# Performance work log

Measured on AMD Instinct MI355X. Metric: run time of the kernel, lower is better.

## Reference

```python
import jax, jax.numpy as jnp
import numpy as np

STRIDES = (8, 16, 32, 64, 128)
IMG = 1024
NUM_CLS = 80
SHRINK_RATIO = 0.2
BIG = 1e7  # padding value for area of non-positive locations (matches tf.pad constant)


def _level_targets(boxes, labels, valid, stride):
    """Vectorized per-level target assignment.
    boxes: [B,M,4] float, labels: [B,M] int32, valid: [B,M] bool.
    Replaces the per-box tf.map_fn + dynamic pad + argmin + gather_nd with a
    dense masked area map and a single argmin/gather pass.
    """
    B, M, _ = boxes.shape
    fh = fw = IMG // stride
    HW = fh * fw
    # shrink_and_normalize_boxes: scale to level, shrink around center, clamp
    b = boxes / stride
    cx = (b[..., 0] + b[..., 2]) * 0.5
    cy = (b[..., 1] + b[..., 3]) * 0.5
    hw = (b[..., 2] - b[..., 0]) * 0.5 * SHRINK_RATIO
    hh = (b[..., 3] - b[..., 1]) * 0.5 * SHRINK_RATIO
    px1 = jnp.maximum(jnp.floor(cx - hw), 0.0)
    py1 = jnp.maximum(jnp.floor(cy - hh), 0.0)
    px2 = jnp.minimum(jnp.ceil(cx + hw), float(fw))
    py2 = jnp.minimum(jnp.ceil(cy + hh), float(fh))
    xs = jnp.arange(fw, dtype=jnp.float32)
    ys = jnp.arange(fh, dtype=jnp.float32)
    in_x = (xs[None, None, None, :] >= px1[:, :, None, None]) & (xs[None, None, None, :] < px2[:, :, None, None])
    in_y = (ys[None, None, :, None] >= py1[:, :, None, None]) & (ys[None, None, :, None] < py2[:, :, None, None])
    inside = in_x & in_y & valid[:, :, None, None]  # [B,M,fh,fw]
    area = (boxes[..., 2] - boxes[..., 0]) * (boxes[..., 3] - boxes[..., 1])  # [B,M]
    area_map = jnp.where(inside, area[:, :, None, None], BIG)  # [B,M,fh,fw]
    winner = jnp.argmin(area_map, axis=1).reshape(B, HW)  # min-area box per pixel
    win_area = jnp.min(area_map, axis=1).reshape(B, HW)
    pos = win_area < BIG  # pixel covered by at least one valid box
    posf = pos.astype(jnp.float32)
    wb = jnp.take_along_axis(boxes, winner[..., None], axis=1)  # [B,HW,4]
    wl = jnp.take_along_axis(labels, winner, axis=1)            # [B,HW]
    yy, xx = jnp.meshgrid(ys, xs, indexing='ij')
    sx = (xx.reshape(-1) + 0.5) * stride  # [HW] anchor-point x in image coords
    sy = (yy.reshape(-1) + 0.5) * stride
    l = sx[None, :] - wb[..., 0]
    t = sy[None, :] - wb[..., 1]
    r = wb[..., 2] - sx[None, :]
    btm = wb[..., 3] - sy[None, :]
    reg = jnp.stack([l, t, r, btm], axis=-1) / (4.0 * stride)  # [B,HW,4]
    eps = 1e-6
    cent = jnp.sqrt(
        jnp.clip(jnp.minimum(l, r) / jnp.maximum(jnp.maximum(l, r), eps), 0.0, 1.0)
        * jnp.clip(jnp.minimum(t, btm) / jnp.maximum(jnp.maximum(t, btm), eps), 0.0, 1.0))
    soft = jnp.where(pos, cent, 1.0)  # negatives padded with 1 (constant_values=1)
    cls_onehot = jax.nn.one_hot(wl, NUM_CLS, dtype=jnp.float32) * posf[..., None]
    cls_t = jnp.concatenate([cls_onehot, soft[..., None], posf[..., None]], axis=-1)  # [B,HW,C+2]
    reg_t = jnp.concatenate([reg * posf[..., None], soft[..., None], posf[..., None]], axis=-1)  # [B,HW,6]
    ind = jnp.where(pos, winner, -1).astype(jnp.int32)
    return cls_t, reg_t, ind


def setup_inputs():
    key = jax.random.key(0)
    B, M = 16, 100
    k1, k2, k3, k4, k5, k6 = jax.random.split(key, 6)
    w = jax.random.uniform(k1, (B, M)) * 240.0 + 16.0
    h = jax.random.uniform(k2, (B, M)) * 240.0 + 16.0
    cx = jax.random.uniform(k3, (B, M)) * (IMG - 260.0) + 130.0
    cy = jax.random.uniform(k4, (B, M)) * (IMG - 260.0) + 130.0
    labels = jax.random.randint(k5, (B, M), 0, NUM_CLS).astype(jnp.float32)
    x1 = cx - w * 0.5
    x2 = cx + w * 0.5
    y1 = cy - h * 0.5
    y2 = cy + h * 0.5
    # zero-pad trailing boxes per batch element (trim_zero_padding_boxes convention)
    n_valid = jax.random.randint(k6, (B,), 10, M + 1)
    valid = jnp.arange(M)[None, :] < n_valid[:, None]
    gt_boxes = jnp.stack([x1, y1, x2, y2, labels], axis=-1) * valid[..., None]
    return {"gt_boxes": gt_boxes.astype(jnp.float32)}


def reference(gt_boxes):
    boxes = gt_boxes[..., :4]
    labels = gt_boxes[..., 4].astype(jnp.int32)
    valid = jnp.sum(jnp.abs(boxes), axis=-1) > 0.0  # trim_zero_padding_boxes
    cls_all, reg_all, ind_all = [], [], []
    for stride in STRIDES:  # fixed 5 FPN levels
        c, r, i = _level_targets(boxes, labels, valid, stride)
        cls_all.append(c)
        reg_all.append(r)
        ind_all.append(i)
    cls_t = jnp.concatenate(cls_all, axis=1)   # [B, 21824, 82]
    reg_t = jnp.concatenate(reg_all, axis=1)   # [B, 21824, 6]
    ind_t = jnp.concatenate(ind_all, axis=1)[..., None]  # [B, 21824, 1]
    num_boxes = jnp.sum(valid.astype(jnp.int32), axis=1, keepdims=True)  # [B,1]
    return cls_t, reg_t, ind_t, num_boxes
```

## Files before the change

### kernel.cpp

```cpp
#include <hip/hip_runtime.h>
#include <stdint.h>

#define NCLS   80
#define HWTOT  21824
#define MBOX   100

#define REG_OFF 28633088ull
#define IND_OFF 30728192ull
#define NB_OFF  31077376ull

__global__ __launch_bounds__(256)
void sapd_targets(const float* __restrict__ gt, float* __restrict__ out)
{
    const int tid = threadIdx.x;
    const int c   = blockIdx.x;
    const int b   = blockIdx.y;

    int lvl, pix0, base;
    if      (c < 64) { lvl = 0; pix0 = c << 8;        base = 0;     }
    else if (c < 80) { lvl = 1; pix0 = (c - 64) << 8; base = 16384; }
    else if (c < 84) { lvl = 2; pix0 = (c - 80) << 8; base = 20480; }
    else if (c < 85) { lvl = 3; pix0 = 0;             base = 21504; }
    else             { lvl = 4; pix0 = 0;             base = 21760; }

    const int   l2fw   = 7 - lvl;
    const int   fw     = 1 << l2fw;
    const float fs     = (float)(8 << lvl);
    const int   chunkN = (lvl == 4) ? 64 : 256;

    const size_t rowbase = (size_t)b * HWTOT + base + pix0;

    __shared__ uint32_t sBB[MBOX];
    __shared__ float    sArea[MBOX];
    __shared__ int      sValid[MBOX];
    __shared__ float4   sBox[MBOX];
    __shared__ int      sLab[MBOX];
    __shared__ float2   sCull[MBOX];
    __shared__ int      sOrig[MBOX];
    __shared__ int      sN;
    __shared__ float4   sMeta[257];
    __shared__ float    rReg[256 * 4];

    if (tid < MBOX) {
        const float* g = gt + ((size_t)b * MBOX + tid) * 5;
        float x1 = g[0], y1 = g[1], x2 = g[2], y2 = g[3], lab = g[4];
        int valid = (fabsf(x1) + fabsf(y1) + fabsf(x2) + fabsf(y2)) > 0.0f;
        float area = (x2 - x1) * (y2 - y1);
        float bx1 = x1 / fs, by1 = y1 / fs, bx2 = x2 / fs, by2 = y2 / fs;
        float cx = (bx1 + bx2) * 0.5f, cy = (by1 + by2) * 0.5f;
        float hw = (bx2 - bx1) * 0.5f * 0.2f, hh = (by2 - by1) * 0.5f * 0.2f;
        float px1 = fmaxf(floorf(cx - hw), 0.0f);
        float py1 = fmaxf(floorf(cy - hh), 0.0f);
        float px2 = fminf(ceilf(cx + hw), (float)fw);
        float py2 = fminf(ceilf(cy + hh), (float)fw);
        uint32_t bb = (uint32_t)px1 | ((uint32_t)py1 << 8) |
                      ((uint32_t)px2 << 16) | ((uint32_t)py2 << 24);
        sBB[tid]    = bb;
        sArea[tid]  = area;
        sValid[tid] = valid;
        sBox[tid]   = make_float4(x1, y1, x2, y2);
        sLab[tid]   = (int)lab;
    }
    __syncthreads();

    if (lvl == 4 && tid == 64) {
        int cnt = 0;
        for (int m = 0; m < MBOX; ++m) cnt += sValid[m];
        out[NB_OFF + b] = (float)cnt;
    }

    if (tid < 64) {
        const int lane = tid;
        const int ry0 = pix0 >> l2fw;
        const int ry1 = ry0 + (chunkN >> l2fw);
        int n0;
        {
            int m = lane;
            uint32_t bb = sBB[m];
            int ix1 = bb & 255, iy1 = (bb >> 8) & 255, ix2 = (bb >> 16) & 255, iy2 = bb >> 24;
            bool pred = sValid[m] && (ix2 > ix1) && (iy2 > ry0) && (iy1 < ry1);
            unsigned long long mk = __ballot(pred);
            n0 = __popcll(mk);
            if (pred) {
                int p = __popcll(mk & ((1ull << lane) - 1ull));
                sCull[p] = make_float2(__uint_as_float(bb), sArea[m]);
                sOrig[p] = m;
            }
        }
        {
            int m = 64 + lane;
            bool pred = false;
            uint32_t bb = 0;
            float ar = 0.0f;
            if (m < MBOX) {
                bb = sBB[m]; ar = sArea[m];
                int ix1 = bb & 255, iy1 = (bb >> 8) & 255, ix2 = (bb >> 16) & 255, iy2 = bb >> 24;
                pred = sValid[m] && (ix2 > ix1) && (iy2 > ry0) && (iy1 < ry1);
            }
            unsigned long long mk = __ballot(pred);
            if (pred) {
                int p = n0 + __popcll(mk & ((1ull << lane) - 1ull));
                sCull[p] = make_float2(__uint_as_float(bb), ar);
                sOrig[p] = m;
            }
            if (lane == 0) sN = n0 + __popcll(mk);
        }
    }
    __syncthreads();

    if (tid < chunkN) {
        const int p  = pix0 + tid;
        const int px = p & (fw - 1);
        const int py = p >> l2fw;
        float bestA = 1e30f; int bestI = -1;
        const int n = sN;
        for (int i = 0; i < n; ++i) {
            float2 e = sCull[i];
            uint32_t bb = __float_as_uint(e.x);
            int x1 = bb & 255, y1 = (bb >> 8) & 255, x2 = (bb >> 16) & 255, y2 = bb >> 24;
            bool hit = (px >= x1) & (px < x2) & (py >= y1) & (py < y2);
            bool upd = hit & (e.y < bestA);
            bestA = upd ? e.y : bestA;
            bestI = upd ? i : bestI;
        }
        bool pos = bestI >= 0;
        int orig = pos ? sOrig[bestI] : 0;
        float4 bx = sBox[orig];
        float sx = ((float)px + 0.5f) * fs;
        float sy = ((float)py + 0.5f) * fs;
        float l  = sx - bx.x, t = sy - bx.y, r = bx.z - sx, bt = bx.w - sy;
        float inv4s = 1.0f / (4.0f * fs);
        float posf  = pos ? 1.0f : 0.0f;
        const float eps = 1e-6f;
        float a1 = fminf(l, r) / fmaxf(fmaxf(l, r), eps);
        a1 = fminf(fmaxf(a1, 0.0f), 1.0f);
        float a2 = fminf(t, bt) / fmaxf(fmaxf(t, bt), eps);
        a2 = fminf(fmaxf(a2, 0.0f), 1.0f);
        float cent = sqrtf(a1 * a2);
        float soft = pos ? cent : 1.0f;
        int   tgt  = pos ? sLab[orig] : 0x7fffffff;
        sMeta[tid] = make_float4(soft, posf, __int_as_float(tgt), 0.0f);
        rReg[tid * 4 + 0] = l  * inv4s * posf;
        rReg[tid * 4 + 1] = t  * inv4s * posf;
        rReg[tid * 4 + 2] = r  * inv4s * posf;
        rReg[tid * 4 + 3] = bt * inv4s * posf;
        out[IND_OFF + rowbase + tid] = pos ? (float)orig : -1.0f;
    }
    __syncthreads();

    {
        float4* o4 = (float4*)(out + rowbase * 82);
        const int n4 = (chunkN * 82) >> 2;
        for (int i = tid; i < n4; i += 256) {
            const int id   = i << 2;
            const unsigned row = (unsigned)id / 82u;
            const int col0 = id - (int)row * 82;
            float4 m1 = sMeta[row];
            float4 m2 = sMeta[row + 1];
            const bool wrap = (col0 == 80);
            const int tgt1 = __float_as_int(m1.z);
            float v0 = (col0 < 80) ? ((col0 == tgt1) ? 1.0f : 0.0f) : m1.x;
            const int c1 = col0 + 1;
            float v1 = (c1 < 80) ? ((c1 == tgt1) ? 1.0f : 0.0f) : m1.y;
            float soft2 = wrap ? m2.x : m1.x;
            float posf2 = wrap ? m2.y : m1.y;
            int   tgt2  = __float_as_int(wrap ? m2.z : m1.z);
            const int c2 = wrap ? 0 : col0 + 2;
            const int c3 = wrap ? 1 : col0 + 3;
            float v2 = (c2 < 80) ? ((c2 == tgt2) ? 1.0f : 0.0f)
                                 : ((c2 == 80) ? soft2 : posf2);
            float v3 = (c3 < 80) ? ((c3 == tgt2) ? 1.0f : 0.0f)
                                 : ((c3 == 80) ? soft2 : posf2);
            o4[i] = make_float4(v0, v1, v2, v3);
        }
    }

    {
        float4* o4 = (float4*)(out + REG_OFF + rowbase * 6);
        const int n4 = (chunkN * 6) >> 2;
        for (int i = tid; i < n4; i += 256) {
            int idx = i << 2;
            float v[4];
            #pragma unroll
            for (int k = 0; k < 4; ++k) {
                int id  = idx + k;
                int row = (int)((unsigned)id / 6u);
                int col = id - row * 6;
                float4 m = sMeta[row];
                v[k] = (col < 4) ? rReg[row * 4 + col] : ((col == 4) ? m.x : m.y);
            }
            o4[i] = make_float4(v[0], v[1], v[2], v[3]);
        }
    }
}

extern "C" void kernel_launch(void* const* d_in, const int* in_sizes, int n_in,
                              void* d_out, int out_size, void* d_ws, size_t ws_size,
                              hipStream_t stream)
{
    const float* gt = (const float*)d_in[0];
    float* out = (float*)d_out;
    sapd_targets<<<dim3(86, 16), 256, 0, stream>>>(gt, out);
}
```

Before: 127.1 us.

## Split target kernel into per-pixel meta pass and grid-wide expand pass

The single kernel is split in two. The first computes per-pixel metadata (soft score, positive flag, label, regression deltas) and writes it to workspace. The second is a grid-stride kernel over 2048 blocks that expands this into the dense 82-column class tensor and the 6-column regression tensor. The aim is to spread the large output write across many more blocks than the 1376-block grid, which had only 256 threads each. The cost is an extra kernel launch and a workspace round trip of about 11 MB.

New measurement: 138.4 us. +8.9%, slower.

```diff
diff --git a/kernel.cpp b/kernel.cpp
--- a/kernel.cpp
+++ b/kernel.cpp
@@ -4,13 +4,18 @@
 #define NCLS   80
 #define HWTOT  21824
 #define MBOX   100
+#define ROWS   349184
 
 #define REG_OFF 28633088ull
 #define IND_OFF 30728192ull
 #define NB_OFF  31077376ull
 
+#define N4C 7158272
+#define N4R 523776
+
 __global__ __launch_bounds__(256)
-void sapd_targets(const float* __restrict__ gt, float* __restrict__ out)
+void sapd_meta(const float* __restrict__ gt, float* __restrict__ out,
+               float4* __restrict__ m0, float4* __restrict__ m1)
 {
     const int tid = threadIdx.x;
     const int c   = blockIdx.x;
@@ -38,8 +43,6 @@
     __shared__ float2   sCull[MBOX];
     __shared__ int      sOrig[MBOX];
     __shared__ int      sN;
-    __shared__ float4   sMeta[257];
-    __shared__ float    rReg[256 * 4];
 
     if (tid < MBOX) {
         const float* g = gt + ((size_t)b * MBOX + tid) * 5;
@@ -139,58 +142,57 @@
         float cent = sqrtf(a1 * a2);
         float soft = pos ? cent : 1.0f;
         int   tgt  = pos ? sLab[orig] : 0x7fffffff;
-        sMeta[tid] = make_float4(soft, posf, __int_as_float(tgt), 0.0f);
-        rReg[tid * 4 + 0] = l  * inv4s * posf;
-        rReg[tid * 4 + 1] = t  * inv4s * posf;
-        rReg[tid * 4 + 2] = r  * inv4s * posf;
-        rReg[tid * 4 + 3] = bt * inv4s * posf;
-        out[IND_OFF + rowbase + tid] = pos ? (float)orig : -1.0f;
-    }
-    __syncthreads();
-
-    {
-        float4* o4 = (float4*)(out + rowbase * 82);
-        const int n4 = (chunkN * 82) >> 2;
-        for (int i = tid; i < n4; i += 256) {
-            const int id   = i << 2;
-            const unsigned row = (unsigned)id / 82u;
-            const int col0 = id - (int)row * 82;
-            float4 m1 = sMeta[row];
-            float4 m2 = sMeta[row + 1];
-            const bool wrap = (col0 == 80);
-            const int tgt1 = __float_as_int(m1.z);
-            float v0 = (col0 < 80) ? ((col0 == tgt1) ? 1.0f : 0.0f) : m1.x;
-            const int c1 = col0 + 1;
-            float v1 = (c1 < 80) ? ((c1 == tgt1) ? 1.0f : 0.0f) : m1.y;
-            float soft2 = wrap ? m2.x : m1.x;
-            float posf2 = wrap ? m2.y : m1.y;
-            int   tgt2  = __float_as_int(wrap ? m2.z : m1.z);
-            const int c2 = wrap ? 0 : col0 + 2;
-            const int c3 = wrap ? 1 : col0 + 3;
-            float v2 = (c2 < 80) ? ((c2 == tgt2) ? 1.0f : 0.0f)
-                                 : ((c2 == 80) ? soft2 : posf2);
-            float v3 = (c3 < 80) ? ((c3 == tgt2) ? 1.0f : 0.0f)
-                                 : ((c3 == 80) ? soft2 : posf2);
-            o4[i] = make_float4(v0, v1, v2, v3);
-        }
-    }
-
-    {
-        float4* o4 = (float4*)(out + REG_OFF + rowbase * 6);
-        const int n4 = (chunkN * 6) >> 2;
-        for (int i = tid; i < n4; i += 256) {
-            int idx = i << 2;
-            float v[4];
-            #pragma unroll
-            for (int k = 0; k < 4; ++k) {
-                int id  = idx + k;
-                int row = (int)((unsigned)id / 6u);
-                int col = id - row * 6;
-                float4 m = sMeta[row];
-                v[k] = (col < 4) ? rReg[row * 4 + col] : ((col == 4) ? m.x : m.y);
-            }
-            o4[i] = make_float4(v[0], v[1], v[2], v[3]);
-        }
+        const size_t grow = rowbase + tid;
+        m0[grow] = make_float4(soft, posf, __int_as_float(tgt), 0.0f);
+        m1[grow] = make_float4(l * inv4s * posf, t * inv4s * posf,
+                               r * inv4s * posf, bt * inv4s * posf);
+        out[IND_OFF + grow] = pos ? (float)orig : -1.0f;
+    }
+}
+
+__global__ __launch_bounds__(256)
+void sapd_expand(const float4* __restrict__ m0, const float4* __restrict__ m1,
+                 float* __restrict__ out)
+{
+    const int gtid   = blockIdx.x * 256 + threadIdx.x;
+    const int stride = gridDim.x * 256;
+
+    float4* oc = (float4*)out;
+    for (int i = gtid; i < N4C; i += stride) {
+        const int id   = i << 2;
+        const unsigned row = (unsigned)id / 82u;
+        const int col0 = id - (int)row * 82;
+        const bool wrap = (col0 == 80);
+        float4 ma = m0[row];
+        float4 mb = m0[row + (wrap ? 1 : 0)];
+        const int tgt1 = __float_as_int(ma.z);
+        float v0 = (col0 < 80) ? ((col0 == tgt1) ? 1.0f : 0.0f) : ma.x;
+        const int c1 = col0 + 1;
+        float v1 = (c1 < 80) ? ((c1 == tgt1) ? 1.0f : 0.0f) : ma.y;
+        const int tgt2 = __float_as_int(mb.z);
+        const int c2 = wrap ? 0 : col0 + 2;
+        const int c3 = wrap ? 1 : col0 + 3;
+        float v2 = (c2 < 80) ? ((c2 == tgt2) ? 1.0f : 0.0f)
+                             : ((c2 == 80) ? mb.x : mb.y);
+        float v3 = (c3 < 80) ? ((c3 == tgt2) ? 1.0f : 0.0f)
+                             : ((c3 == 80) ? mb.x : mb.y);
+        oc[i] = make_float4(v0, v1, v2, v3);
+    }
+
+    float4* orr = (float4*)(out + REG_OFF);
+    for (int i = gtid; i < N4R; i += stride) {
+        const int id   = i << 2;
+        const unsigned row = (unsigned)id / 6u;
+        const int col0 = id - (int)row * 6;
+        const bool w4 = (col0 == 4);
+        float4 a  = m0[row];
+        float4 rg = m1[row];
+        float4 r2 = m1[row + (w4 ? 1 : 0)];
+        float4 v;
+        if (col0 == 0)      v = rg;
+        else if (col0 == 2) v = make_float4(rg.z, rg.w, a.x, a.y);
+        else                v = make_float4(a.x, a.y, r2.x, r2.y);
+        orr[i] = v;
     }
 }
 
@@ -200,5 +202,8 @@
 {
     const float* gt = (const float*)d_in[0];
     float* out = (float*)d_out;
-    sapd_targets<<<dim3(86, 16), 256, 0, stream>>>(gt, out);
+    float4* m0 = (float4*)d_ws;
+    float4* m1 = m0 + ROWS;
+    sapd_meta<<<dim3(86, 16), 256, 0, stream>>>(gt, out, m0, m1);
+    sapd_expand<<<2048, 256, 0, stream>>>(m0, m1, out);
 }
```
